# Performance work log

Measured on AMD Instinct MI355X. Metric: run time of the kernel, lower is better.

## Reference

```python
import jax, jax.numpy as jnp
import numpy as np

S, B, I, H = 512, 8192, 3, 5  # seq, batch, input_size, hidden_size


def _uniform(key, shape, bound):
    return jax.random.uniform(key, shape, jnp.float32, -bound, bound)


def setup_inputs() -> dict:
    key = jax.random.key(0)
    ks = jax.random.split(key, 17)
    bound = 1.0 / np.sqrt(H)
    inp = {"x": jax.random.normal(ks[0], (S, B, I), jnp.float32)}
    # layer 0: in=I ; layer 1: in=2H (concat of both directions). Suffix 'r' = reverse direction.
    specs = [
        ("l0", I), ("l0r", I), ("l1", 2 * H), ("l1r", 2 * H),
    ]
    ki = 1
    for name, din in specs:
        inp[f"w_ih_{name}"] = _uniform(ks[ki], (4 * H, din), bound); ki += 1
        inp[f"w_hh_{name}"] = _uniform(ks[ki], (4 * H, H), bound); ki += 1
        inp[f"b_ih_{name}"] = _uniform(ks[ki], (4 * H,), bound); ki += 1
        inp[f"b_hh_{name}"] = _uniform(ks[ki], (4 * H,), bound); ki += 1
    return inp


def _lstm_dir(x, w_ih, w_hh, b_ih, b_hh, reverse):
    """Single-direction LSTM over x [S,B,Din] -> (hs [S,B,H], h_T [B,H], c_T [B,H])."""
    xs = x[::-1] if reverse else x
    # Precompute input contributions for all timesteps in one big matmul.
    gx = jnp.einsum('sbi,gi->sbg', xs, w_ih) + b_ih + b_hh  # [S,B,4H]
    h0 = jnp.zeros((x.shape[1], H), x.dtype)
    c0 = jnp.zeros((x.shape[1], H), x.dtype)

    def step(carry, g):
        h, c = carry
        g = g + h @ w_hh.T  # [B,4H]
        i, f, gg, o = jnp.split(g, 4, axis=-1)  # PyTorch gate order: i,f,g,o
        i = jax.nn.sigmoid(i)
        f = jax.nn.sigmoid(f)
        gg = jnp.tanh(gg)
        o = jax.nn.sigmoid(o)
        c = f * c + i * gg
        h = o * jnp.tanh(c)
        return (h, c), h

    (hT, cT), hs = jax.lax.scan(step, (h0, c0), gx)
    if reverse:
        hs = hs[::-1]
    return hs, hT, cT


def reference(x,
              w_ih_l0, w_hh_l0, b_ih_l0, b_hh_l0,
              w_ih_l0r, w_hh_l0r, b_ih_l0r, b_hh_l0r,
              w_ih_l1, w_hh_l1, b_ih_l1, b_hh_l1,
              w_ih_l1r, w_hh_l1r, b_ih_l1r, b_hh_l1r):
    # Layer 0 (bidirectional)
    hs0f, h0f, c0f = _lstm_dir(x, w_ih_l0, w_hh_l0, b_ih_l0, b_hh_l0, False)
    hs0b, h0b, c0b = _lstm_dir(x, w_ih_l0r, w_hh_l0r, b_ih_l0r, b_hh_l0r, True)
    out0 = jnp.concatenate([hs0f, hs0b], axis=-1)  # [S,B,2H]
    # Layer 1 (bidirectional) consumes concat of both directions
    hs1f, h1f, c1f = _lstm_dir(out0, w_ih_l1, w_hh_l1, b_ih_l1, b_hh_l1, False)
    hs1b, h1b, c1b = _lstm_dir(out0, w_ih_l1r, w_hh_l1r, b_ih_l1r, b_hh_l1r, True)
    output = jnp.concatenate([hs1f, hs1b], axis=-1)  # [S,B,2H]
    # PyTorch h_n/c_n layout: [num_layers*num_directions, B, H] ordered (l0 fwd, l0 bwd, l1 fwd, l1 bwd)
    h_n = jnp.stack([h0f, h0b, h1f, h1b], axis=0)
    c_n = jnp.stack([c0f, c0b, c1f, c1b], axis=0)
    return output, h_n, c_n
```

## Files before the change

kernel.cpp:

```cpp
#include <hip/hip_runtime.h>


constexpr int S_ = 512;
constexpr int B_ = 8192;
constexpr int NROW = 16384;

constexpr int GD1  = 1366;
constexpr int TL   = 208;
constexpr int GSTR = GD1 * 64;

constexpr float L2E  = 1.4426950408889634f;
constexpr float T2E  = 2.8853900817779268f;
constexpr float IT2E = 0.34657359027997264f;

typedef _Float16 v2h __attribute__((ext_vector_type(2)));

__device__ __forceinline__ float dot2h(v2h a, v2h b, float c) {
#if __has_builtin(__builtin_amdgcn_fdot2)
    return __builtin_amdgcn_fdot2(a, b, c, false);
#else
    return fmaf((float)a[0], (float)b[0], fmaf((float)a[1], (float)b[1], c));
#endif
}

__device__ __forceinline__ float rcp_(float x) { return __builtin_amdgcn_rcpf(x); }

__device__ __forceinline__ float exp2_(float x) {
#if __has_builtin(__builtin_amdgcn_exp2f)
    return __builtin_amdgcn_exp2f(x);
#else
    return exp2f(x);
#endif
}

__device__ __forceinline__ void sbar() { __builtin_amdgcn_sched_barrier(0); }

__device__ __forceinline__ float bperm(int bidx, float v) {
    return __int_as_float(__builtin_amdgcn_ds_bpermute(bidx, __float_as_int(v)));
}

__device__ __forceinline__ unsigned pkh(float a, float b) {
    auto t = __builtin_amdgcn_cvt_pkrtz(a, b);
    unsigned q; __builtin_memcpy(&q, &t, 4); return q;
}

__device__ __forceinline__ unsigned short f2h(float x) {
    _Float16 h = (_Float16)x;
    unsigned short s; __builtin_memcpy(&s, &h, 2); return s;
}

__device__ __forceinline__ float h2f(unsigned short s) {
    _Float16 h; __builtin_memcpy(&h, &s, 2); return (float)h;
}

__global__ __launch_bounds__(64) __attribute__((amdgpu_waves_per_eu(1, 2)))
void lstm_layer0(
    const float* __restrict__ x,
    const float* __restrict__ wih_f, const float* __restrict__ whh_f,
    const float* __restrict__ bih_f, const float* __restrict__ bhh_f,
    const float* __restrict__ wih_r, const float* __restrict__ whh_r,
    const float* __restrict__ bih_r, const float* __restrict__ bhh_r,
    unsigned short* __restrict__ ws,
    float* __restrict__ outbase)
{
    const int l64 = threadIdx.x & 63;
    int r = l64 / 5; r = (r > 11) ? 11 : r;
    const int u   = l64 - r * 5;
    const int uc  = (u < 5) ? u : 4;
    const int gid = blockIdx.x * 12 + r;
    const bool valid = gid < NROW;
    const int dir = (gid >> 13) & 1;
    const int b   = gid & 8191;
    const bool stw = valid && (u < 3);
    const bool st  = valid && (u < 5);

    int bidx[5];
#pragma unroll
    for (int k = 0; k < 5; k++) bidx[k] = (r * 5 + k) * 4;

    const float* __restrict__ wih = dir ? wih_r : wih_f;
    const float* __restrict__ whh = dir ? whh_r : whh_f;
    const float* __restrict__ bih = dir ? bih_r : bih_f;
    const float* __restrict__ bhh = dir ? bhh_r : bhh_f;

    const int rows[4] = {uc, 5 + uc, 10 + uc, 15 + uc};
    const float scl[4] = {-L2E, -L2E, T2E, -L2E};
    float WX[4][3], WH[4][5], BS[4];
#pragma unroll
    for (int gi = 0; gi < 4; gi++) {
        const int rr = rows[gi]; const float sc = scl[gi];
#pragma unroll
        for (int i = 0; i < 3; i++) WX[gi][i] = wih[rr * 3 + i] * sc;
#pragma unroll
        for (int k = 0; k < 5; k++) WH[gi][k] = whh[rr * 5 + k] * sc;
        BS[gi] = (bih[rr] + bhh[rr]) * sc;
    }

    float h[5] = {0.f, 0.f, 0.f, 0.f, 0.f};
    float cp = 0.f, hu_last = 0.f;

    const int t0 = dir ? (S_ - 1) : 0;
    const float* xp = x + ((size_t)t0 * B_ + b) * 3;
    unsigned short* wp = ws + (size_t)dir * ((size_t)S_ * B_ * 6)
                            + ((size_t)t0 * B_ + b) * 6;
    const ptrdiff_t xst = dir ? -(ptrdiff_t)3 * B_ : (ptrdiff_t)3 * B_;
    const ptrdiff_t wst = dir ? -(ptrdiff_t)6 * B_ : (ptrdiff_t)6 * B_;

    auto step = [&](const float (&xin)[3], unsigned short* wpp) {
        float a0 = BS[0], a1 = BS[1], a2 = BS[2], a3 = BS[3];
#pragma unroll
        for (int i = 0; i < 3; i++) {
            a0 = fmaf(WX[0][i], xin[i], a0);
            a1 = fmaf(WX[1][i], xin[i], a1);
            a2 = fmaf(WX[2][i], xin[i], a2);
            a3 = fmaf(WX[3][i], xin[i], a3);
        }
#pragma unroll
        for (int k = 0; k < 5; k++) {
            a0 = fmaf(WH[0][k], h[k], a0);
            a1 = fmaf(WH[1][k], h[k], a1);
            a2 = fmaf(WH[2][k], h[k], a2);
            a3 = fmaf(WH[3][k], h[k], a3);
        }
        const float ig = rcp_(1.0f + exp2_(a0));
        const float fg = rcp_(1.0f + exp2_(a1));
        const float g2 = fmaf(-2.0f * T2E, rcp_(1.0f + exp2_(a2)), T2E);
        const float og = rcp_(1.0f + exp2_(a3));
        cp = fmaf(fg, cp, ig * g2);
        const float th = fmaf(-2.0f, rcp_(1.0f + exp2_(cp)), 1.0f);
        const float hu = og * th;
        hu_last = hu;
#pragma unroll
        for (int k = 0; k < 5; k++) h[k] = bperm(bidx[k], hu);
        const unsigned q0 = pkh(h[0], h[1]);
        const unsigned q1 = pkh(h[2], h[3]);
        const unsigned q2 = pkh(h[4], 0.0f);
        unsigned qs = q0;
        qs = (u == 1) ? q1 : qs;
        qs = (u == 2) ? q2 : qs;
        if (stw) ((unsigned*)wpp)[u] = qs;
    };

    auto ld = [&](float (&buf)[3]) {
        __builtin_memcpy(&buf[0], xp, 12);
        xp += xst;
        sbar();
    };

    float x0[3], x1[3], x2[3], x3[3], x4[3], x5[3], x6[3], x7[3];
    ld(x0); ld(x1); ld(x2); ld(x3); ld(x4); ld(x5); ld(x6); ld(x7);

#pragma unroll 1
    for (int s = 0; s < S_ - 8; s += 8) {
        step(x0, wp); wp += wst; ld(x0);
        step(x1, wp); wp += wst; ld(x1);
        step(x2, wp); wp += wst; ld(x2);
        step(x3, wp); wp += wst; ld(x3);
        step(x4, wp); wp += wst; ld(x4);
        step(x5, wp); wp += wst; ld(x5);
        step(x6, wp); wp += wst; ld(x6);
        step(x7, wp); wp += wst; ld(x7);
    }
    step(x0, wp); wp += wst;
    step(x1, wp); wp += wst;
    step(x2, wp); wp += wst;
    step(x3, wp); wp += wst;
    step(x4, wp); wp += wst;
    step(x5, wp); wp += wst;
    step(x6, wp); wp += wst;
    step(x7, wp);

    const size_t OUTE = (size_t)S_ * B_ * 10;
    float* hn = outbase + OUTE + ((size_t)dir * B_ + b) * 5;
    float* cn = hn + (size_t)4 * B_ * 5;
    if (st) { hn[uc] = hu_last; cn[uc] = cp * IT2E; }
}

__global__ __launch_bounds__(64) __attribute__((amdgpu_waves_per_eu(1, 2)))
void lstm_layer1(
    const unsigned short* __restrict__ ws,
    const float* __restrict__ wih_f, const float* __restrict__ whh_f,
    const float* __restrict__ bih_f, const float* __restrict__ bhh_f,
    const float* __restrict__ wih_r, const float* __restrict__ whh_r,
    const float* __restrict__ bih_r, const float* __restrict__ bhh_r,
    float* __restrict__ outbase,
    unsigned short* __restrict__ gtemp)
{
    __shared__ unsigned short lt[TL * 60];

    const int l64 = threadIdx.x & 63;
    int r = l64 / 5; r = (r > 11) ? 11 : r;
    const int u   = l64 - r * 5;
    const int uc  = (u < 5) ? u : 4;
    const int rm  = (r < 6) ? r : r - 6;
    const int dir = (r >= 6) ? 1 : 0;
    const int braw = blockIdx.x * 6 + rm;
    const bool valid = braw < B_;
    const int b   = valid ? braw : (B_ - 1);
    const bool st = valid && (u < 5);
    const bool lw = (l64 < 60);
    const int dir5 = dir * 5;
    const int pslot = (dir ? (r - 6) : (r + 6)) * 5 + uc;

    int bidx[5];
#pragma unroll
    for (int k = 0; k < 5; k++) bidx[k] = (r * 5 + k) * 4;

    const float* __restrict__ wih = dir ? wih_r : wih_f;
    const float* __restrict__ whh = dir ? whh_r : whh_f;
    const float* __restrict__ bih = dir ? bih_r : bih_f;
    const float* __restrict__ bhh = dir ? bhh_r : bhh_f;

    const int rows[4] = {uc, 5 + uc, 10 + uc, 15 + uc};
    const float scl[4] = {-L2E, -L2E, T2E, -L2E};
    v2h WX[4][6];
    float WH[4][5], BS[4];
#pragma unroll
    for (int gi = 0; gi < 4; gi++) {
        const int rr = rows[gi]; const float sc = scl[gi];
#pragma unroll
        for (int p = 0; p < 6; p++) {
            const int i0 = (p < 3) ? 2 * p : 2 * p - 1;
            const bool pad = (p == 2) || (p == 5);
            const float w0 = wih[rr * 10 + i0] * sc;
            const float w1 = pad ? 0.f : wih[rr * 10 + i0 + 1] * sc;
            WX[gi][p] = (v2h){(_Float16)w0, (_Float16)w1};
        }
#pragma unroll
        for (int k = 0; k < 5; k++) WH[gi][k] = whh[rr * 5 + k] * sc;
        BS[gi] = (bih[rr] + bhh[rr]) * sc;
    }

    float h[5] = {0.f, 0.f, 0.f, 0.f, 0.f};
    float cp = 0.f, hu_last = 0.f;

    const int t0 = dir ? (S_ - 1) : 0;
    const unsigned short* rpf = ws + ((size_t)t0 * B_ + b) * 6;
    const unsigned short* rpb = rpf + (size_t)S_ * B_ * 6;
    float* op = outbase + ((size_t)(dir ? 255 : 256) * B_ + b) * 10;
    const ptrdiff_t rst = dir ? -(ptrdiff_t)6 * B_ : (ptrdiff_t)6 * B_;
    const ptrdiff_t ost = dir ? -(ptrdiff_t)10 * B_ : (ptrdiff_t)10 * B_;

    unsigned short* gw = gtemp + (size_t)blockIdx.x * 64 + l64;
    const unsigned short* gr = gtemp + (size_t)47 * GSTR
                                     + (size_t)blockIdx.x * 64 + pslot;

    auto core = [&](const v2h (&xin)[6]) -> float {
        float a0 = BS[0], a1 = BS[1], a2 = BS[2], a3 = BS[3];
#pragma unroll
        for (int p = 0; p < 6; p++) {
            a0 = dot2h(xin[p], WX[0][p], a0);
            a1 = dot2h(xin[p], WX[1][p], a1);
            a2 = dot2h(xin[p], WX[2][p], a2);
            a3 = dot2h(xin[p], WX[3][p], a3);
        }
#pragma unroll
        for (int k = 0; k < 5; k++) {
            a0 = fmaf(WH[0][k], h[k], a0);
            a1 = fmaf(WH[1][k], h[k], a1);
            a2 = fmaf(WH[2][k], h[k], a2);
            a3 = fmaf(WH[3][k], h[k], a3);
        }
        const float ig = rcp_(1.0f + exp2_(a0));
        const float fg = rcp_(1.0f + exp2_(a1));
        const float g2 = fmaf(-2.0f * T2E, rcp_(1.0f + exp2_(a2)), T2E);
        const float og = rcp_(1.0f + exp2_(a3));
        cp = fmaf(fg, cp, ig * g2);
        const float th = fmaf(-2.0f, rcp_(1.0f + exp2_(cp)), 1.0f);
        const float hu = og * th;
        hu_last = hu;
        return hu;
    };

    auto bcast = [&](float hu) {
#pragma unroll
        for (int k = 0; k < 5; k++) h[k] = bperm(bidx[k], hu);
    };

    auto step1L = [&](const v2h (&xin)[6], int t) {
        const float hu = core(xin);
        if (lw) lt[t * 60 + l64] = f2h(hu);
        bcast(hu);
    };
    auto step1G = [&](const v2h (&xin)[6]) {
        const float hu = core(xin);
        *gw = f2h(hu);
        gw += GSTR;
        bcast(hu);
    };
    auto step2G = [&](const v2h (&xin)[6], float* opp) {
        const float pv = h2f(*gr);
        gr -= GSTR;
        const float hu = core(xin);
        if (st) { opp[dir5 + u] = hu; opp[5 - dir5 + u] = pv; }
        bcast(hu);
    };
    auto step2L = [&](const v2h (&xin)[6], int t, float* opp) {
        const float pv = h2f(lt[(511 - t) * 60 + pslot]);
        const float hu = core(xin);
        if (st) { opp[dir5 + u] = hu; opp[5 - dir5 + u] = pv; }
        bcast(hu);
    };

    auto ld = [&](v2h (&buf)[6]) {
        __builtin_memcpy(&buf[0], rpf, 12);
        __builtin_memcpy(&buf[3], rpb, 12);
        rpf += rst; rpb += rst;
        sbar();
    };

    v2h x0[6], x1[6], x2[6], x3[6];
    ld(x0); ld(x1); ld(x2); ld(x3);

#pragma unroll 1
    for (int t = 0; t < TL; t += 4) {
        step1L(x0, t + 0); ld(x0);
        step1L(x1, t + 1); ld(x1);
        step1L(x2, t + 2); ld(x2);
        step1L(x3, t + 3); ld(x3);
    }
#pragma unroll 1
    for (int t = TL; t < 256; t += 4) {
        step1G(x0); ld(x0);
        step1G(x1); ld(x1);
        step1G(x2); ld(x2);
        step1G(x3); ld(x3);
    }
#pragma unroll 1
    for (int t = 256; t < 304; t += 4) {
        step2G(x0, op); op += ost; ld(x0);
        step2G(x1, op); op += ost; ld(x1);
        step2G(x2, op); op += ost; ld(x2);
        step2G(x3, op); op += ost; ld(x3);
    }
#pragma unroll 1
    for (int t = 304; t < 508; t += 4) {
        step2L(x0, t + 0, op); op += ost; ld(x0);
        step2L(x1, t + 1, op); op += ost; ld(x1);
        step2L(x2, t + 2, op); op += ost; ld(x2);
        step2L(x3, t + 3, op); op += ost; ld(x3);
    }
    step2L(x0, 508, op); op += ost;
    step2L(x1, 509, op); op += ost;
    step2L(x2, 510, op); op += ost;
    step2L(x3, 511, op);

    const size_t OUTE = (size_t)S_ * B_ * 10;
    float* hn = outbase + OUTE + ((size_t)(2 + dir) * B_ + b) * 5;
    float* cn = hn + (size_t)4 * B_ * 5;
    if (st) { hn[uc] = hu_last; cn[uc] = cp * IT2E; }
}

extern "C" void kernel_launch(void* const* d_in, const int* in_sizes, int n_in,
                              void* d_out, int out_size, void* d_ws, size_t ws_size,
                              hipStream_t stream) {
    const float* x       = (const float*)d_in[0];
    const float* wih_l0  = (const float*)d_in[1];
    const float* whh_l0  = (const float*)d_in[2];
    const float* bih_l0  = (const float*)d_in[3];
    const float* bhh_l0  = (const float*)d_in[4];
    const float* wih_l0r = (const float*)d_in[5];
    const float* whh_l0r = (const float*)d_in[6];
    const float* bih_l0r = (const float*)d_in[7];
    const float* bhh_l0r = (const float*)d_in[8];
    const float* wih_l1  = (const float*)d_in[9];
    const float* whh_l1  = (const float*)d_in[10];
    const float* bih_l1  = (const float*)d_in[11];
    const float* bhh_l1  = (const float*)d_in[12];
    const float* wih_l1r = (const float*)d_in[13];
    const float* whh_l1r = (const float*)d_in[14];
    const float* bih_l1r = (const float*)d_in[15];
    const float* bhh_l1r = (const float*)d_in[16];

    float* out = (float*)d_out;
    unsigned short* ws = (unsigned short*)d_ws;
    unsigned short* gtemp = ws + (size_t)2 * S_ * B_ * 6;

    dim3 grid0(1366), block(64);
    lstm_layer0<<<grid0, block, 0, stream>>>(x,
        wih_l0, whh_l0, bih_l0, bhh_l0,
        wih_l0r, whh_l0r, bih_l0r, bhh_l0r,
        ws, out);
    dim3 grid1(GD1);
    lstm_layer1<<<grid1, block, 0, stream>>>(ws,
        wih_l1, whh_l1, bih_l1, bhh_l1,
        wih_l1r, whh_l1r, bih_l1r, bhh_l1r,
        out, gtemp);
}
```

Measured before the change: 330.8 us.

## Remap layer-1 lanes to 8-lane groups with 4 batches per block

Layer-1 now gives each wave 4 batch elements per direction in 8-lane groups (5 active) instead of 6 per direction in 5-lane groups. That doubles the grid to 2048 blocks and allows 2-4 waves per EU, to improve occupancy and latency hiding on the serial recurrence. The LDS history buffer grows to 240 steps with a narrower stride, so fewer steps spill to the global temp buffer. Global temp reads are now prefetched four steps ahead. The cost is idle lanes (40 of 64 active instead of 60), a shifted gtemp base, and tighter register limits that may cause spills.

```diff
diff --git a/kernel.cpp b/kernel.cpp
--- a/kernel.cpp
+++ b/kernel.cpp
@@ -5,8 +5,8 @@
 constexpr int B_ = 8192;
 constexpr int NROW = 16384;
 
-constexpr int GD1  = 1366;
-constexpr int TL   = 208;
+constexpr int GD1  = 2048;
+constexpr int TL   = 240;
 constexpr int GSTR = GD1 * 64;
 
 constexpr float L2E  = 1.4426950408889634f;
@@ -176,7 +176,7 @@
     if (st) { hn[uc] = hu_last; cn[uc] = cp * IT2E; }
 }
 
-__global__ __launch_bounds__(64) __attribute__((amdgpu_waves_per_eu(1, 2)))
+__global__ __launch_bounds__(64) __attribute__((amdgpu_waves_per_eu(2, 4)))
 void lstm_layer1(
     const unsigned short* __restrict__ ws,
     const float* __restrict__ wih_f, const float* __restrict__ whh_f,
@@ -186,25 +186,24 @@
     float* __restrict__ outbase,
     unsigned short* __restrict__ gtemp)
 {
-    __shared__ unsigned short lt[TL * 60];
+    __shared__ unsigned short lt[TL * 40];
 
     const int l64 = threadIdx.x & 63;
-    int r = l64 / 5; r = (r > 11) ? 11 : r;
-    const int u   = l64 - r * 5;
-    const int uc  = (u < 5) ? u : 4;
-    const int rm  = (r < 6) ? r : r - 6;
-    const int dir = (r >= 6) ? 1 : 0;
-    const int braw = blockIdx.x * 6 + rm;
-    const bool valid = braw < B_;
-    const int b   = valid ? braw : (B_ - 1);
-    const bool st = valid && (u < 5);
-    const bool lw = (l64 < 60);
+    const int r  = l64 >> 3;
+    const int u  = l64 & 7;
+    const int uc = (u < 5) ? u : 4;
+    const int rm  = r & 3;
+    const int dir = r >> 2;
+    const int b   = blockIdx.x * 4 + rm;
+    const bool st = (u < 5);
     const int dir5 = dir * 5;
-    const int pslot = (dir ? (r - 6) : (r + 6)) * 5 + uc;
+    const int pr  = dir ? (r - 4) : (r + 4);
+    const int psL = pr * 5 + uc;
+    const int psG = pr * 8 + uc;
 
     int bidx[5];
 #pragma unroll
-    for (int k = 0; k < 5; k++) bidx[k] = (r * 5 + k) * 4;
+    for (int k = 0; k < 5; k++) bidx[k] = (r * 8 + k) * 4;
 
     const float* __restrict__ wih = dir ? wih_r : wih_f;
     const float* __restrict__ whh = dir ? whh_r : whh_f;
@@ -242,8 +241,8 @@
     const ptrdiff_t ost = dir ? -(ptrdiff_t)10 * B_ : (ptrdiff_t)10 * B_;
 
     unsigned short* gw = gtemp + (size_t)blockIdx.x * 64 + l64;
-    const unsigned short* gr = gtemp + (size_t)47 * GSTR
-                                     + (size_t)blockIdx.x * 64 + pslot;
+    const unsigned short* gr = gtemp + (size_t)15 * GSTR
+                                     + (size_t)blockIdx.x * 64 + psG;
 
     auto core = [&](const v2h (&xin)[6]) -> float {
         float a0 = BS[0], a1 = BS[1], a2 = BS[2], a3 = BS[3];
@@ -279,7 +278,7 @@
 
     auto step1L = [&](const v2h (&xin)[6], int t) {
         const float hu = core(xin);
-        if (lw) lt[t * 60 + l64] = f2h(hu);
+        if (st) lt[t * 40 + r * 5 + u] = f2h(hu);
         bcast(hu);
     };
     auto step1G = [&](const v2h (&xin)[6]) {
@@ -288,15 +287,14 @@
         gw += GSTR;
         bcast(hu);
     };
-    auto step2G = [&](const v2h (&xin)[6], float* opp) {
-        const float pv = h2f(*gr);
-        gr -= GSTR;
+    auto step2G = [&](const v2h (&xin)[6], unsigned short pvs, float* opp) {
+        const float pv = h2f(pvs);
         const float hu = core(xin);
         if (st) { opp[dir5 + u] = hu; opp[5 - dir5 + u] = pv; }
         bcast(hu);
     };
     auto step2L = [&](const v2h (&xin)[6], int t, float* opp) {
-        const float pv = h2f(lt[(511 - t) * 60 + pslot]);
+        const float pv = h2f(lt[(511 - t) * 40 + psL]);
         const float hu = core(xin);
         if (st) { opp[dir5 + u] = hu; opp[5 - dir5 + u] = pv; }
         bcast(hu);
@@ -326,15 +324,20 @@
         step1G(x2); ld(x2);
         step1G(x3); ld(x3);
     }
-#pragma unroll 1
-    for (int t = 256; t < 304; t += 4) {
-        step2G(x0, op); op += ost; ld(x0);
-        step2G(x1, op); op += ost; ld(x1);
-        step2G(x2, op); op += ost; ld(x2);
-        step2G(x3, op); op += ost; ld(x3);
-    }
-#pragma unroll 1
-    for (int t = 304; t < 508; t += 4) {
+    asm volatile("s_waitcnt vmcnt(0)" ::: "memory");
+    unsigned short pva = *gr; gr -= GSTR;
+    unsigned short pvb = *gr; gr -= GSTR;
+    unsigned short pvc = *gr; gr -= GSTR;
+    unsigned short pvd = *gr; gr -= GSTR;
+#pragma unroll 1
+    for (int t = 256; t < 272; t += 4) {
+        step2G(x0, pva, op); op += ost; pva = *gr; gr -= GSTR; ld(x0);
+        step2G(x1, pvb, op); op += ost; pvb = *gr; gr -= GSTR; ld(x1);
+        step2G(x2, pvc, op); op += ost; pvc = *gr; gr -= GSTR; ld(x2);
+        step2G(x3, pvd, op); op += ost; pvd = *gr; gr -= GSTR; ld(x3);
+    }
+#pragma unroll 1
+    for (int t = 272; t < 508; t += 4) {
         step2L(x0, t + 0, op); op += ost; ld(x0);
         step2L(x1, t + 1, op); op += ost; ld(x1);
         step2L(x2, t + 2, op); op += ost; ld(x2);
@@ -348,7 +351,7 @@
     const size_t OUTE = (size_t)S_ * B_ * 10;
     float* hn = outbase + OUTE + ((size_t)(2 + dir) * B_ + b) * 5;
     float* cn = hn + (size_t)4 * B_ * 5;
-    if (st) { hn[uc] = hu_last; cn[uc] = cp * IT2E; }
+    if (st) { hn[u] = hu_last; cn[u] = cp * IT2E; }
 }
 
 extern "C" void kernel_launch(void* const* d_in, const int* in_sizes, int n_in,
@@ -374,7 +377,7 @@
 
     float* out = (float*)d_out;
     unsigned short* ws = (unsigned short*)d_ws;
-    unsigned short* gtemp = ws + (size_t)2 * S_ * B_ * 6;
+    unsigned short* gtemp = ws + (size_t)2 * S_ * B_ * 6 + (size_t)4 * GSTR;
 
     dim3 grid0(1366), block(64);
     lstm_layer0<<<grid0, block, 0, stream>>>(x,
```

Result: no change. 327.5 us (-1.0%).
